# Performance work log

Hardware: AMD Instinct MI355X
Metric: run time of the kernel (lower is better)

Reference implementation:

```python
import jax, jax.numpy as jnp
import numpy as np

L_MAX = 3
N_RADIAL = [2, 2, 1, 1]  # radial powers r^{2k} with 2k+l <= l_max=3


def fibonacci_sphere(n):
    i = np.arange(n, dtype=np.float64)
    phi = np.pi * (3.0 - np.sqrt(5.0))
    y = 1.0 - 2.0 * i / (n - 1)
    r = np.sqrt(np.maximum(1.0 - y * y, 0.0))
    th = phi * i
    pts = np.stack([np.cos(th) * r, y, np.sin(th) * r], -1)
    return jnp.asarray(pts, dtype=jnp.float32)


def real_sh(u):
    # real spherical harmonics on unit vectors u[...,3], degrees 0..3
    x, y, z = u[..., 0], u[..., 1], u[..., 2]
    Y0 = 0.28209479 * jnp.ones_like(x)[..., None]
    Y1 = 0.48860251 * jnp.stack([y, z, x], -1)
    Y2 = jnp.stack([
        1.09254843 * x * y,
        1.09254843 * y * z,
        0.31539157 * (3.0 * z * z - 1.0),
        1.09254843 * x * z,
        0.54627421 * (x * x - y * y)], -1)
    Y3 = jnp.stack([
        0.59004359 * y * (3.0 * x * x - y * y),
        2.89061144 * x * y * z,
        0.45704579 * y * (5.0 * z * z - 1.0),
        0.37317633 * z * (5.0 * z * z - 3.0),
        0.45704579 * x * (5.0 * z * z - 1.0),
        1.44530572 * z * (x * x - y * y),
        0.59004359 * x * (x * x - 3.0 * y * y)], -1)
    return [Y0, Y1, Y2, Y3]


def grid_sample_3d(vol, grid):
    # vol: [B, D, H, W]; grid: [B, d, h, w, 3], grid[...,0]->W, [...,1]->H, [...,2]->D
    # align_corners=True, zeros padding (torch.nn.functional.grid_sample semantics)
    B, Dv, Hv, Wv = vol.shape
    ix = (grid[..., 0] + 1.0) * 0.5 * (Wv - 1)
    iy = (grid[..., 1] + 1.0) * 0.5 * (Hv - 1)
    iz = (grid[..., 2] + 1.0) * 0.5 * (Dv - 1)
    x0f, y0f, z0f = jnp.floor(ix), jnp.floor(iy), jnp.floor(iz)
    wx, wy, wz = ix - x0f, iy - y0f, iz - z0f
    x0, y0, z0 = x0f.astype(jnp.int32), y0f.astype(jnp.int32), z0f.astype(jnp.int32)
    x1, y1, z1 = x0 + 1, y0 + 1, z0 + 1
    bidx = jnp.arange(B).reshape(B, 1, 1, 1)

    def tap(zi, yi, xi):
        m = ((zi >= 0) & (zi < Dv) & (yi >= 0) & (yi < Hv) & (xi >= 0) & (xi < Wv)).astype(vol.dtype)
        v = vol[bidx, jnp.clip(zi, 0, Dv - 1), jnp.clip(yi, 0, Hv - 1), jnp.clip(xi, 0, Wv - 1)]
        return v * m

    out = (tap(z0, y0, x0) * (1 - wz) * (1 - wy) * (1 - wx)
         + tap(z0, y0, x1) * (1 - wz) * (1 - wy) * wx
         + tap(z0, y1, x0) * (1 - wz) * wy * (1 - wx)
         + tap(z0, y1, x1) * (1 - wz) * wy * wx
         + tap(z1, y0, x0) * wz * (1 - wy) * (1 - wx)
         + tap(z1, y0, x1) * wz * (1 - wy) * wx
         + tap(z1, y1, x0) * wz * wy * (1 - wx)
         + tap(z1, y1, x1) * wz * wy * wx)
    return out


def setup_inputs() -> dict:
    key = jax.random.key(0)
    ks = jax.random.split(key, 12)
    B, H, W, D, S = 8, 32, 32, 32, 64
    x = jax.random.normal(ks[0], (B, H, W, D, 3), jnp.float32) * 0.35
    x_density = jax.random.uniform(ks[1], (B, H, W, D), jnp.float32)
    F = jax.random.normal(ks[2], (B, S, 256), jnp.float32) * 0.1
    def lin(k, i, o):
        return jax.random.normal(k, (i, o), jnp.float32) / np.sqrt(i)
    return {
        'x': x, 'x_density': x_density, 'F': F,
        'S2': fibonacci_sphere(S),
        'bw1': lin(ks[3], 256, 64), 'bb1': jnp.zeros((64,), jnp.float32),
        'bw2': lin(ks[4], 64, 3), 'bb2': jnp.zeros((3,), jnp.float32),
        'cw1': lin(ks[5], 256, 128), 'cb1': jnp.zeros((128,), jnp.float32),
        'cw2': lin(ks[6], 128, 64), 'cb2': jnp.zeros((64,), jnp.float32),
        'iw': lin(ks[7], 128, 3), 'ib': jnp.zeros((3,), jnp.float32),
    }


def reference(x, x_density, F, S2, bw1, bb1, bw2, bb2, cw1, cb1, cw2, cb2, iw, ib):
    B, H, W, D, _ = x.shape
    S = S2.shape[0]
    quad = (4.0 * jnp.pi) / S  # sphere quadrature weight for fibonacci samples
    Ybase = real_sh(S2)  # list of [S, 2l+1]

    # frame (E) branch: basis MLP -> type-1 SH coefficients -> normalize
    basis = jax.nn.relu(F @ bw1 + bb1) @ bw2 + bb2          # [B,S,3]
    E = jnp.einsum('vm,bvc->bmc', Ybase[1], basis) * quad   # [B,3,3]
    E = E / jnp.clip(jnp.linalg.norm(E, axis=-1, keepdims=True), 1e-6)

    # latent code branch: code MLP -> full SHT coefficients per degree l
    latent = jax.nn.relu(F @ cw1 + cb1) @ cw2 + cb2         # [B,S,64]
    coeffs = [jnp.einsum('vm,bvc->bmc', Ybase[l], latent) * quad for l in range(L_MAX + 1)]

    # zernike monomials of the grid points
    xf = x.reshape(B, -1, 3)                                # [B,V,3]
    r = jnp.linalg.norm(xf, axis=-1, keepdims=True)         # [B,V,1]
    u = xf / jnp.clip(r, 1e-6)
    Yx = real_sh(u)
    points_code = []
    points_inv = None
    for l in range(L_MAX + 1):
        Pl = Yx[l] * (r ** l)                               # solid harmonic [B,V,2l+1]
        rad = jnp.stack([r[..., 0] ** (2 * k) for k in range(N_RADIAL[l])], -1)  # [B,V,n_l]
        zl = Pl[..., :, None] * rad[..., None, :]           # [B,V,2l+1,n_l]
        p = jnp.einsum('bmi,bvmj->bvij', coeffs[l], zl)     # [B,V,64,n_l]
        p = p.reshape(B, p.shape[1], -1)
        points_code.append(p)
        if l == 1:
            points_inv = p                                  # [B,V,128]
    points_code = jnp.concatenate(points_code, -1)          # [B,V,384]

    pts = points_inv @ iw + ib                              # [B,V,3]
    coords = pts.reshape(B, H, W, D, 3)
    vol = x_density.reshape(B, H, W, D)
    sampled = grid_sample_3d(vol, coords)                   # [B,H,W,D]
    return sampled, E, coords, points_code
```

## Files before the change

kernel.cpp:

```cpp
#include <hip/hip_runtime.h>
#include <math.h>

#define OFF_E     262144
#define OFF_COORD 262216
#define OFF_CODE  1048648

#define QUAD 0.19634954084936207f

#define WS_H1 0
#define WS_H2 32768
#define WS_C  98304
#define WS_AB 106496

typedef float f4v __attribute__((ext_vector_type(4)));

__global__ __launch_bounds__(384) void k_hidden(
    const float* __restrict__ F,
    const float* __restrict__ bw1, const float* __restrict__ bb1,
    const float* __restrict__ cw1, const float* __restrict__ cb1,
    float* __restrict__ ws)
{
    __shared__ float sF[8 * 257];
    const int blk = blockIdx.x;
    const int b   = blk >> 3;
    const int r0  = (blk & 7) * 8;
    const int tid = threadIdx.x;

    float* wsH1 = ws + WS_H1;
    float* wsH2 = ws + WS_H2;

    const float* Fb = F + ((size_t)b * 64 + r0) * 256;
    for (int i = tid; i < 2048; i += 384) sF[(i >> 8) * 257 + (i & 255)] = Fb[i];
    __syncthreads();

    if (tid < 128) {
        const int row = tid >> 4, k4 = (tid & 15) * 4;
        const float* fr = sF + row * 257;
        float4 acc = *(const float4*)&bb1[k4];
        #pragma unroll 4
        for (int j = 0; j < 256; ++j) {
            const float  f = fr[j];
            const float4 w = *(const float4*)&bw1[j * 64 + k4];
            acc.x = fmaf(f, w.x, acc.x);
            acc.y = fmaf(f, w.y, acc.y);
            acc.z = fmaf(f, w.z, acc.z);
            acc.w = fmaf(f, w.w, acc.w);
        }
        acc.x = fmaxf(acc.x, 0.f); acc.y = fmaxf(acc.y, 0.f);
        acc.z = fmaxf(acc.z, 0.f); acc.w = fmaxf(acc.w, 0.f);
        *(float4*)&wsH1[((size_t)b * 64 + r0 + row) * 64 + k4] = acc;
    } else {
        const int tt  = tid - 128;
        const int row = tt >> 5, k4 = (tt & 31) * 4;
        const float* fr = sF + row * 257;
        float4 acc = *(const float4*)&cb1[k4];
        #pragma unroll 4
        for (int j = 0; j < 256; ++j) {
            const float  f = fr[j];
            const float4 w = *(const float4*)&cw1[j * 128 + k4];
            acc.x = fmaf(f, w.x, acc.x);
            acc.y = fmaf(f, w.y, acc.y);
            acc.z = fmaf(f, w.z, acc.z);
            acc.w = fmaf(f, w.w, acc.w);
        }
        acc.x = fmaxf(acc.x, 0.f); acc.y = fmaxf(acc.y, 0.f);
        acc.z = fmaxf(acc.z, 0.f); acc.w = fmaxf(acc.w, 0.f);
        *(float4*)&wsH2[((size_t)b * 64 + r0 + row) * 128 + k4] = acc;
    }
}

__global__ __launch_bounds__(512) void k_coeffs(
    const float* __restrict__ ws_in,
    const float* __restrict__ S2,
    const float* __restrict__ bw2, const float* __restrict__ bb2,
    const float* __restrict__ cw2, const float* __restrict__ cb2,
    const float* __restrict__ iw,
    float* __restrict__ ws_out, float* __restrict__ outE)
{
    __shared__ float sH2[64 * 129];
    __shared__ alignas(16) float sLat[64 * 64];
    __shared__ float sY[64 * 16];
    __shared__ float sBas[64 * 3];
    __shared__ float sC[16 * 64];
    __shared__ float sE[9];

    const int b = blockIdx.x, tid = threadIdx.x;
    const float* wsH1 = ws_in + WS_H1;
    const float* wsH2 = ws_in + WS_H2;
    float* wsC  = ws_out + WS_C;
    float* wsAB = ws_out + WS_AB;

    const float* H2b = wsH2 + (size_t)b * 8192;
    for (int i = tid; i < 8192; i += 512) sH2[(i >> 7) * 129 + (i & 127)] = H2b[i];

    if (tid < 64) {
        const float x = S2[tid * 3 + 0], y = S2[tid * 3 + 1], z = S2[tid * 3 + 2];
        float* Yv = sY + tid * 16;
        Yv[0]  = 0.28209479f;
        Yv[1]  = 0.48860251f * y;
        Yv[2]  = 0.48860251f * z;
        Yv[3]  = 0.48860251f * x;
        Yv[4]  = 1.09254843f * x * y;
        Yv[5]  = 1.09254843f * y * z;
        Yv[6]  = 0.31539157f * (3.f * z * z - 1.f);
        Yv[7]  = 1.09254843f * x * z;
        Yv[8]  = 0.54627421f * (x * x - y * y);
        Yv[9]  = 0.59004359f * y * (3.f * x * x - y * y);
        Yv[10] = 2.89061144f * x * y * z;
        Yv[11] = 0.45704579f * y * (5.f * z * z - 1.f);
        Yv[12] = 0.37317633f * z * (5.f * z * z - 3.f);
        Yv[13] = 0.45704579f * x * (5.f * z * z - 1.f);
        Yv[14] = 1.44530572f * z * (x * x - y * y);
        Yv[15] = 0.59004359f * x * (x * x - 3.f * y * y);
    }

    float breg = 0.f;
    if (tid < 192) {
        const int v = tid / 3, c = tid % 3;
        const float* h1 = wsH1 + ((size_t)b * 64 + v) * 64;
        float acc = bb2[c];
        #pragma unroll 8
        for (int k = 0; k < 64; ++k) acc = fmaf(h1[k], bw2[k * 3 + c], acc);
        breg = acc;
    }
    __syncthreads();

    if (tid < 192) sBas[tid] = breg;

    for (int t = tid; t < 1024; t += 512) {
        const int row = t >> 4, i4 = (t & 15) * 4;
        const float* h2 = sH2 + row * 129;
        float4 acc = *(const float4*)&cb2[i4];
        #pragma unroll 4
        for (int k = 0; k < 128; ++k) {
            const float  h = h2[k];
            const float4 w = *(const float4*)&cw2[k * 64 + i4];
            acc.x = fmaf(h, w.x, acc.x);
            acc.y = fmaf(h, w.y, acc.y);
            acc.z = fmaf(h, w.z, acc.z);
            acc.w = fmaf(h, w.w, acc.w);
        }
        *(float4*)&sLat[row * 64 + i4] = acc;
    }
    __syncthreads();

    for (int o = tid; o < 1024; o += 512) {
        const int m = o >> 6, i = o & 63;
        float acc = 0.f;
        #pragma unroll 8
        for (int v = 0; v < 64; ++v) acc = fmaf(sY[v * 16 + m], sLat[v * 64 + i], acc);
        acc *= QUAD;
        sC[o] = acc;
        wsC[(size_t)b * 1024 + o] = acc;
    }
    if (tid < 9) {
        const int m = tid / 3, c = tid % 3;
        float acc = 0.f;
        for (int v = 0; v < 64; ++v) acc = fmaf(sY[v * 16 + 1 + m], sBas[v * 3 + c], acc);
        sE[tid] = acc * QUAD;
    }
    __syncthreads();

    if (tid < 9) {
        const int m = tid / 3;
        const float e0 = sE[m * 3 + 0], e1 = sE[m * 3 + 1], e2 = sE[m * 3 + 2];
        const float n = sqrtf(e0 * e0 + e1 * e1 + e2 * e2);
        outE[b * 9 + tid] = sE[tid] / fmaxf(n, 1e-6f);
    }
    if (tid < 18) {
        const int which = tid / 9, mc = tid % 9;
        const int m = mc / 3, c = mc % 3;
        float acc = 0.f;
        #pragma unroll 8
        for (int i = 0; i < 64; ++i)
            acc = fmaf(sC[(1 + m) * 64 + i], iw[(2 * i + which) * 3 + c], acc);
        wsAB[b * 18 + tid] = acc;
    }
}

__global__ __launch_bounds__(384) void k_code(
    const float* __restrict__ x, const float* __restrict__ dens,
    const float* __restrict__ ws, const float* __restrict__ ib,
    float* __restrict__ out)
{
    __shared__ alignas(16) float sC[1024];
    __shared__ alignas(16) float sT[64 * 32];

    const int blk   = blockIdx.x;
    const int b     = blk & 7;
    const int vbase = (blk >> 3) * 64;
    const int tid   = threadIdx.x;

    if (tid < 256)
        ((f4v*)sC)[tid] = ((const f4v*)(ws + WS_C + b * 1024))[tid];

    if (tid < 64) {
        const int g = b * 32768 + vbase + tid;
        const float px = x[(size_t)g * 3 + 0];
        const float py = x[(size_t)g * 3 + 1];
        const float pz = x[(size_t)g * 3 + 2];
        const float r2 = px * px + py * py + pz * pz;
        const float r   = sqrtf(r2);
        const float inv = 1.f / fmaxf(r, 1e-6f);
        const float ux = px * inv, uy = py * inv, uz = pz * inv;
        const float r3 = r2 * r;

        const float z1 = 0.48860251f * uy * r;
        const float z2 = 0.48860251f * uz * r;
        const float z3 = 0.48860251f * ux * r;

        float* T = sT + tid * 32;
        T[0]  = 1.f;  T[1] = r2;  T[2] = 0.f; T[3] = 0.f;
        T[4]  = 0.f;  T[5] = 0.f; T[6] = 0.f; T[7] = 0.f;
        T[8]  = z1;   T[9] = z2;  T[10] = z3;
        T[11] = z1 * r2; T[12] = z2 * r2; T[13] = z3 * r2;
        T[14] = 0.f;  T[15] = 0.f;
        T[16] = 1.09254843f * ux * uy * r2;
        T[17] = 1.09254843f * uy * uz * r2;
        T[18] = 0.31539157f * (3.f * uz * uz - 1.f) * r2;
        T[19] = 1.09254843f * ux * uz * r2;
        T[20] = 0.54627421f * (ux * ux - uy * uy) * r2;
        T[21] = 0.f; T[22] = 0.f; T[23] = 0.f;
        T[24] = 0.59004359f * uy * (3.f * ux * ux - uy * uy) * r3;
        T[25] = 2.89061144f * ux * uy * uz * r3;
        T[26] = 0.45704579f * uy * (5.f * uz * uz - 1.f) * r3;
        T[27] = 0.37317633f * uz * (5.f * uz * uz - 3.f) * r3;
        T[28] = 0.45704579f * ux * (5.f * uz * uz - 1.f) * r3;
        T[29] = 1.44530572f * uz * (ux * ux - uy * uy) * r3;
        T[30] = 0.59004359f * ux * (ux * ux - 3.f * uy * uy) * r3;
        T[31] = 0.f;

        const float* AB = ws + WS_AB + b * 18;
        float pt[3];
        #pragma unroll
        for (int cc = 0; cc < 3; ++cc) {
            float acc = ib[cc];
            acc = fmaf(z1, AB[0 + cc] + r2 * AB[9  + cc], acc);
            acc = fmaf(z2, AB[3 + cc] + r2 * AB[12 + cc], acc);
            acc = fmaf(z3, AB[6 + cc] + r2 * AB[15 + cc], acc);
            pt[cc] = acc;
            out[OFF_COORD + (size_t)g * 3 + cc] = acc;
        }
        const float ixf = (pt[0] + 1.f) * 0.5f * 31.f;
        const float iyf = (pt[1] + 1.f) * 0.5f * 31.f;
        const float izf = (pt[2] + 1.f) * 0.5f * 31.f;
        const float x0f = floorf(ixf), y0f = floorf(iyf), z0f = floorf(izf);
        const float wx = ixf - x0f, wy = iyf - y0f, wz = izf - z0f;
        const int x0 = (int)x0f, y0 = (int)y0f, z0 = (int)z0f;
        const float* volb = dens + (size_t)b * 32768;
        float s = 0.f;
        #pragma unroll
        for (int dz = 0; dz < 2; ++dz) {
            const int zi = z0 + dz;
            const float wzz = dz ? wz : 1.f - wz;
            #pragma unroll
            for (int dy = 0; dy < 2; ++dy) {
                const int yi = y0 + dy;
                const float wyy = dy ? wy : 1.f - wy;
                #pragma unroll
                for (int dx = 0; dx < 2; ++dx) {
                    const int xi = x0 + dx;
                    const float wxx = dx ? wx : 1.f - wx;
                    if (zi >= 0 && zi < 32 && yi >= 0 && yi < 32 && xi >= 0 && xi < 32)
                        s += wzz * wyy * wxx * volb[zi * 1024 + yi * 32 + xi];
                }
            }
        }
        out[g] = s;
    }
    __syncthreads();

    const int w  = tid >> 6, l = tid & 63;
    const int g0 = w * 256 + 4 * l;
    const int rw = g0 / 384;
    const int c  = g0 - rw * 384;

    f4v cf0 = {0.f,0.f,0.f,0.f}, cf1 = cf0, cf2 = cf0, cf3 = cf0;
    f4v cf4 = cf0, cf5 = cf0, cf6 = cf0;
    int tb;
    if (c < 128) {
        const int i0 = c >> 1;
        const float ca = sC[i0]     * 0.28209479f;
        const float cb = sC[i0 + 1] * 0.28209479f;
        cf0 = (f4v){ca, 0.f, cb, 0.f};
        cf1 = (f4v){0.f, ca, 0.f, cb};
        tb = 0;
    } else if (c < 256) {
        const int u = (c - 128) >> 1;
        const float a0 = sC[64 + u],     a1 = sC[128 + u],     a2 = sC[192 + u];
        const float b0 = sC[64 + u + 1], b1 = sC[128 + u + 1], b2 = sC[192 + u + 1];
        cf0 = (f4v){a0, 0.f, b0, 0.f};
        cf1 = (f4v){a1, 0.f, b1, 0.f};
        cf2 = (f4v){a2, 0.f, b2, 0.f};
        cf3 = (f4v){0.f, a0, 0.f, b0};
        cf4 = (f4v){0.f, a1, 0.f, b1};
        cf5 = (f4v){0.f, a2, 0.f, b2};
        tb = 8;
    } else if (c < 320) {
        const int i0 = c - 256;
        cf0 = *(const f4v*)&sC[4 * 64 + i0];
        cf1 = *(const f4v*)&sC[5 * 64 + i0];
        cf2 = *(const f4v*)&sC[6 * 64 + i0];
        cf3 = *(const f4v*)&sC[7 * 64 + i0];
        cf4 = *(const f4v*)&sC[8 * 64 + i0];
        tb = 16;
    } else {
        const int i0 = c - 320;
        cf0 = *(const f4v*)&sC[ 9 * 64 + i0];
        cf1 = *(const f4v*)&sC[10 * 64 + i0];
        cf2 = *(const f4v*)&sC[11 * 64 + i0];
        cf3 = *(const f4v*)&sC[12 * 64 + i0];
        cf4 = *(const f4v*)&sC[13 * 64 + i0];
        cf5 = *(const f4v*)&sC[14 * 64 + i0];
        cf6 = *(const f4v*)&sC[15 * 64 + i0];
        tb = 24;
    }

    const float* Tb = sT + tb;
    float* po = out + OFF_CODE + ((size_t)(b * 32768 + vbase)) * 384 + g0;

    #pragma unroll 4
    for (int p = 0; p < 16; ++p) {
        const int ro = (4 * p + rw) * 32;
        const f4v ta = *(const f4v*)(Tb + ro);
        const f4v tb4 = *(const f4v*)(Tb + ro + 4);
        f4v acc = cf0 * ta.x;
        acc += cf1 * ta.y;
        acc += cf2 * ta.z;
        acc += cf3 * ta.w;
        acc += cf4 * tb4.x;
        acc += cf5 * tb4.y;
        acc += cf6 * tb4.z;
        *(f4v*)(po + p * 1536) = acc;
    }
}

extern "C" void kernel_launch(void* const* d_in, const int* in_sizes, int n_in,
                              void* d_out, int out_size, void* d_ws, size_t ws_size,
                              hipStream_t stream) {
    const float* x    = (const float*)d_in[0];
    const float* dens = (const float*)d_in[1];
    const float* F    = (const float*)d_in[2];
    const float* S2   = (const float*)d_in[3];
    const float* bw1  = (const float*)d_in[4];
    const float* bb1  = (const float*)d_in[5];
    const float* bw2  = (const float*)d_in[6];
    const float* bb2  = (const float*)d_in[7];
    const float* cw1  = (const float*)d_in[8];
    const float* cb1  = (const float*)d_in[9];
    const float* cw2  = (const float*)d_in[10];
    const float* cb2  = (const float*)d_in[11];
    const float* iw   = (const float*)d_in[12];
    const float* ib   = (const float*)d_in[13];
    float* out = (float*)d_out;
    float* ws  = (float*)d_ws;

    k_hidden<<<64,   384, 0, stream>>>(F, bw1, bb1, cw1, cb1, ws);
    k_coeffs<<<8,    512, 0, stream>>>(ws, S2, bw2, bb2, cw2, cb2, iw, ws, out + OFF_E);
    k_code<<<4096,   384, 0, stream>>>(x, dens, ws, ib, out);
}
```

Baseline: 503.6 us.

## Warp-specialize code kernel with double-buffered producer wave over four tiles

Each block now handles four 64-point tiles using 448 threads: one dedicated producer wave computes the monomial table, coords and the grid sample for the next tile into a double-buffered shared array, while six consumer waves write the 384-wide code for the current tile. The coefficient registers are loaded once per block instead of once per tile. The aim is to hide the serial per-point setup behind the store-heavy code output and to amortize block setup. The trade-off is fewer blocks and a barrier per tile, and the producer wave may end up as the bottleneck.

```diff
diff --git a/kernel.cpp b/kernel.cpp
--- a/kernel.cpp
+++ b/kernel.cpp
@@ -178,24 +178,25 @@
     }
 }
 
-__global__ __launch_bounds__(384) void k_code(
+__global__ __launch_bounds__(448) void k_code(
     const float* __restrict__ x, const float* __restrict__ dens,
     const float* __restrict__ ws, const float* __restrict__ ib,
     float* __restrict__ out)
 {
     __shared__ alignas(16) float sC[1024];
-    __shared__ alignas(16) float sT[64 * 32];
-
-    const int blk   = blockIdx.x;
-    const int b     = blk & 7;
-    const int vbase = (blk >> 3) * 64;
-    const int tid   = threadIdx.x;
+    __shared__ alignas(16) float sT[2][64 * 32];
+
+    const int blk = blockIdx.x;
+    const int t0  = blk * 4;
+    const int b   = blk >> 7;
+    const int tid = threadIdx.x;
 
     if (tid < 256)
         ((f4v*)sC)[tid] = ((const f4v*)(ws + WS_C + b * 1024))[tid];
 
-    if (tid < 64) {
-        const int g = b * 32768 + vbase + tid;
+    auto produce = [&](int tile, float* Tbuf) {
+        const int ln = tid - 384;
+        const int g  = tile * 64 + ln;
         const float px = x[(size_t)g * 3 + 0];
         const float py = x[(size_t)g * 3 + 1];
         const float pz = x[(size_t)g * 3 + 2];
@@ -209,7 +210,7 @@
         const float z2 = 0.48860251f * uz * r;
         const float z3 = 0.48860251f * ux * r;
 
-        float* T = sT + tid * 32;
+        float* T = Tbuf + ln * 32;
         T[0]  = 1.f;  T[1] = r2;  T[2] = 0.f; T[3] = 0.f;
         T[4]  = 0.f;  T[5] = 0.f; T[6] = 0.f; T[7] = 0.f;
         T[8]  = z1;   T[9] = z2;  T[10] = z3;
@@ -267,71 +268,92 @@
             }
         }
         out[g] = s;
-    }
-    __syncthreads();
-
-    const int w  = tid >> 6, l = tid & 63;
-    const int g0 = w * 256 + 4 * l;
-    const int rw = g0 / 384;
-    const int c  = g0 - rw * 384;
-
+    };
+
+    int tb = 0, rw = 0, g0 = 0;
     f4v cf0 = {0.f,0.f,0.f,0.f}, cf1 = cf0, cf2 = cf0, cf3 = cf0;
     f4v cf4 = cf0, cf5 = cf0, cf6 = cf0;
-    int tb;
-    if (c < 128) {
-        const int i0 = c >> 1;
-        const float ca = sC[i0]     * 0.28209479f;
-        const float cb = sC[i0 + 1] * 0.28209479f;
-        cf0 = (f4v){ca, 0.f, cb, 0.f};
-        cf1 = (f4v){0.f, ca, 0.f, cb};
-        tb = 0;
-    } else if (c < 256) {
-        const int u = (c - 128) >> 1;
-        const float a0 = sC[64 + u],     a1 = sC[128 + u],     a2 = sC[192 + u];
-        const float b0 = sC[64 + u + 1], b1 = sC[128 + u + 1], b2 = sC[192 + u + 1];
-        cf0 = (f4v){a0, 0.f, b0, 0.f};
-        cf1 = (f4v){a1, 0.f, b1, 0.f};
-        cf2 = (f4v){a2, 0.f, b2, 0.f};
-        cf3 = (f4v){0.f, a0, 0.f, b0};
-        cf4 = (f4v){0.f, a1, 0.f, b1};
-        cf5 = (f4v){0.f, a2, 0.f, b2};
-        tb = 8;
-    } else if (c < 320) {
-        const int i0 = c - 256;
-        cf0 = *(const f4v*)&sC[4 * 64 + i0];
-        cf1 = *(const f4v*)&sC[5 * 64 + i0];
-        cf2 = *(const f4v*)&sC[6 * 64 + i0];
-        cf3 = *(const f4v*)&sC[7 * 64 + i0];
-        cf4 = *(const f4v*)&sC[8 * 64 + i0];
-        tb = 16;
-    } else {
-        const int i0 = c - 320;
-        cf0 = *(const f4v*)&sC[ 9 * 64 + i0];
-        cf1 = *(const f4v*)&sC[10 * 64 + i0];
-        cf2 = *(const f4v*)&sC[11 * 64 + i0];
-        cf3 = *(const f4v*)&sC[12 * 64 + i0];
-        cf4 = *(const f4v*)&sC[13 * 64 + i0];
-        cf5 = *(const f4v*)&sC[14 * 64 + i0];
-        cf6 = *(const f4v*)&sC[15 * 64 + i0];
-        tb = 24;
-    }
-
-    const float* Tb = sT + tb;
-    float* po = out + OFF_CODE + ((size_t)(b * 32768 + vbase)) * 384 + g0;
-
-    #pragma unroll 4
-    for (int p = 0; p < 16; ++p) {
-        const int ro = (4 * p + rw) * 32;
-        const f4v ta = *(const f4v*)(Tb + ro);
-        const f4v tb4 = *(const f4v*)(Tb + ro + 4);
-        f4v acc = cf0 * ta.x;
-        acc += cf1 * ta.y;
-        acc += cf2 * ta.z;
-        acc += cf3 * ta.w;
-        acc += cf4 * tb4.x;
-        acc += cf5 * tb4.y;
-        acc += cf6 * tb4.z;
-        *(f4v*)(po + p * 1536) = acc;
+    if (tid < 384) {
+        const int w = tid >> 6, l = tid & 63;
+        g0 = w * 256 + 4 * l;
+        rw = g0 / 384;
+        const int c = g0 - rw * 384;
+
+        if (c < 128) {
+            const int i0 = c >> 1;
+            const float ca = sC[i0]     * 0.28209479f;
+            (void)ca;
+            tb = 0;
+        }
+    }
+
+    if (tid >= 384) produce(t0, sT[0]);
+    __syncthreads();
+
+    if (tid < 384) {
+        const int c = g0 - rw * 384;
+        if (c < 128) {
+            const int i0 = c >> 1;
+            const float ca = sC[i0]     * 0.28209479f;
+            const float cb = sC[i0 + 1] * 0.28209479f;
+            cf0 = (f4v){ca, 0.f, cb, 0.f};
+            cf1 = (f4v){0.f, ca, 0.f, cb};
+            tb = 0;
+        } else if (c < 256) {
+            const int u = (c - 128) >> 1;
+            const float a0 = sC[64 + u],     a1 = sC[128 + u],     a2 = sC[192 + u];
+            const float b0 = sC[64 + u + 1], b1 = sC[128 + u + 1], b2 = sC[192 + u + 1];
+            cf0 = (f4v){a0, 0.f, b0, 0.f};
+            cf1 = (f4v){a1, 0.f, b1, 0.f};
+            cf2 = (f4v){a2, 0.f, b2, 0.f};
+            cf3 = (f4v){0.f, a0, 0.f, b0};
+            cf4 = (f4v){0.f, a1, 0.f, b1};
+            cf5 = (f4v){0.f, a2, 0.f, b2};
+            tb = 8;
+        } else if (c < 320) {
+            const int i0 = c - 256;
+            cf0 = *(const f4v*)&sC[4 * 64 + i0];
+            cf1 = *(const f4v*)&sC[5 * 64 + i0];
+            cf2 = *(const f4v*)&sC[6 * 64 + i0];
+            cf3 = *(const f4v*)&sC[7 * 64 + i0];
+            cf4 = *(const f4v*)&sC[8 * 64 + i0];
+            tb = 16;
+        } else {
+            const int i0 = c - 320;
+            cf0 = *(const f4v*)&sC[ 9 * 64 + i0];
+            cf1 = *(const f4v*)&sC[10 * 64 + i0];
+            cf2 = *(const f4v*)&sC[11 * 64 + i0];
+            cf3 = *(const f4v*)&sC[12 * 64 + i0];
+            cf4 = *(const f4v*)&sC[13 * 64 + i0];
+            cf5 = *(const f4v*)&sC[14 * 64 + i0];
+            cf6 = *(const f4v*)&sC[15 * 64 + i0];
+            tb = 24;
+        }
+    }
+
+    #pragma unroll
+    for (int t = 0; t < 4; ++t) {
+        if (tid >= 384) {
+            if (t < 3) produce(t0 + t + 1, sT[(t + 1) & 1]);
+        } else {
+            const float* Tb = sT[t & 1] + tb;
+            float* po = out + OFF_CODE + (size_t)(t0 + t) * 24576 + g0;
+            #pragma unroll 4
+            for (int p = 0; p < 16; ++p) {
+                const int ro = (4 * p + rw) * 32;
+                const f4v ta  = *(const f4v*)(Tb + ro);
+                const f4v tb4 = *(const f4v*)(Tb + ro + 4);
+                f4v acc = cf0 * ta.x;
+                acc += cf1 * ta.y;
+                acc += cf2 * ta.z;
+                acc += cf3 * ta.w;
+                acc += cf4 * tb4.x;
+                acc += cf5 * tb4.y;
+                acc += cf6 * tb4.z;
+                *(f4v*)(po + p * 1536) = acc;
+            }
+        }
+        __syncthreads();
     }
 }
 
@@ -357,5 +379,5 @@
 
     k_hidden<<<64,   384, 0, stream>>>(F, bw1, bb1, cw1, cb1, ws);
     k_coeffs<<<8,    512, 0, stream>>>(ws, S2, bw2, bb2, cw2, cb2, iw, ws, out + OFF_E);
-    k_code<<<4096,   384, 0, stream>>>(x, dens, ws, ib, out);
+    k_code<<<1024,   448, 0, stream>>>(x, dens, ws, ib, out);
 }
```

New measurement: 503.9 us. No clear change (+0.1%).
